# Kernel tuning notes

Hardware: AMD Instinct MI355X
Metric: run time of the kernel (lower is better)

The kernel has to match this reference:

```python
import jax, jax.numpy as jnp
import numpy as np

B, S, C = 16, 720, 862      # batch, seq_len, enc_in
P = 24                      # highest_freq_period
PAD = 720                   # seq_len % P == 0 -> pad_len == seq_len (no padding branch taken)
LQ = PAD // P               # 30, per-branch subsequence length == conv channels
DM = 128                    # d_model (PECBlock hidden conv channels)
EL = 2                      # e_layers
PRED = 336                  # pred_len
EPS = 1e-5                  # RevIN eps


def setup_inputs() -> dict:
    key = jax.random.key(0)
    ks = jax.random.split(key, 6)
    x = jax.random.normal(ks[0], (B, S, C), jnp.float32)
    # per-layer, per-branch pointwise conv weights (kernel_size=1, no bias)
    W1 = jax.random.normal(ks[1], (EL, P, DM, LQ), jnp.float32) * 0.05   # conv1: LQ -> DM
    W2 = jax.random.normal(ks[2], (EL, P, LQ, DM), jnp.float32) * 0.05   # conv2: DM -> LQ
    proj_w = jax.random.normal(ks[3], (PRED, S), jnp.float32) * 0.02      # Linear(seq_len, pred_len)
    proj_b = jnp.zeros((PRED,), jnp.float32)
    rev_w = jnp.ones((C,), jnp.float32)    # RevIN affine weight
    rev_b = jnp.zeros((C,), jnp.float32)   # RevIN affine bias
    return dict(x=x, W1=W1, W2=W2, proj_w=proj_w, proj_b=proj_b, rev_w=rev_w, rev_b=rev_b)


def reference(x, W1, W2, proj_w, proj_b, rev_w, rev_b):
    # RevIN 'norm': stats over time dim (unbiased=False var), affine
    mean = jnp.mean(x, axis=1, keepdims=True)
    stdev = jnp.sqrt(jnp.var(x, axis=1, keepdims=True) + EPS)
    xn = (x - mean) / stdev * rev_w + rev_b

    # seq_len % P == 0 so pad_time_series is identity
    x_padded = xn
    # NOTE: original loop feeds x_padded into EVERY block (not chained),
    # so each iteration overwrites y; replicated faithfully.
    # Strided gather idx::P == reshape (B,C,LQ,P) and index last axis;
    # scatter reassembly y[:,:,idx::P]=... == reshape back from (B,C,LQ,P).
    xs = x_padded.transpose(0, 2, 1).reshape(B, C, LQ, P)  # (B,C,LQ,P)
    y = x_padded
    for l in range(EL):
        h = jax.nn.gelu(jnp.einsum('pdq,bcqp->pbdc', W1[l], xs), approximate=False)  # (P,B,DM,C)
        ys = jnp.einsum('pqd,pbdc->bcqp', W2[l], h)                                  # (B,C,LQ,P)
        y = ys.reshape(B, C, PAD).transpose(0, 2, 1)                                 # (B,PAD,C)

    # PredictedProjection: Linear over time dim
    out = jnp.einsum('ps,bsc->bpc', proj_w, y[:, :S, :]) + proj_b[None, :, None]  # (B,PRED,C)

    # RevIN 'denorm'
    out = (out - rev_b) / (rev_w + EPS * EPS)
    out = out * stdev + mean
    return out
```

## Files before the change

kernel.cpp:

```cpp
#include <hip/hip_runtime.h>
#include <math.h>

typedef __attribute__((ext_vector_type(8))) short bf16x8;
typedef __attribute__((ext_vector_type(4))) short short4v;
typedef __attribute__((ext_vector_type(4))) float f32x4;

#define NB 16
#define NS 720
#define NC 862
#define NP 24
#define NQ 30
#define NDM 128
#define NPRED 336
#define BC (NB*NC)
#define SCH 10
#define SLEN 72
#define KP 768
#define PBASE (4*BC)
#define WOFF_F (24*BC)
#define NCOL (NB*NC)

__device__ __forceinline__ short f2bf(float f) {
    union { float f; unsigned u; } v; v.f = f;
    unsigned r = v.u + 0x7FFFu + ((v.u >> 16) & 1u);
    return (short)(r >> 16);
}

__device__ __forceinline__ float gelu_f(float h) {
    float hc = fminf(fmaxf(h, -8.f), 8.f);
    float z2 = hc * hc;
    float zz = hc * (0.79788456f + 0.035677408f * z2);
    float e  = __expf(-2.f * zz);
    return h * __builtin_amdgcn_rcpf(1.f + e);
}

__device__ __forceinline__ void gl_lds16(const void* g, void* l) {
    __builtin_amdgcn_global_load_lds(
        (const __attribute__((address_space(1))) unsigned int*)g,
        (__attribute__((address_space(3))) unsigned int*)l, 16, 0, 0);
}

__global__ __launch_bounds__(256) void stats_partial_k(const float* __restrict__ x,
                                                       float* __restrict__ ws) {
    int b = blockIdx.x, ct = blockIdx.y, ch = blockIdx.z;
    int c = ct * 256 + threadIdx.x;
    if (c >= NC) return;
    const float* xp = x + ((size_t)b * NS + (size_t)ch * SLEN) * NC + c;
    float s = 0.f, sq = 0.f;
    #pragma unroll 4
    for (int i = 0; i < SLEN; ++i) {
        float v = xp[(size_t)i * NC];
        s += v; sq += v * v;
    }
    int idx = b * NC + c;
    float* ps = ws + PBASE;
    ps[(size_t)ch * BC + idx] = s;
    ps[(size_t)(SCH + ch) * BC + idx] = sq;
}

__global__ __launch_bounds__(256) void stats_final_k(float* __restrict__ ws,
                                                     const float* __restrict__ revw,
                                                     const float* __restrict__ revb) {
    int idx = blockIdx.x * 256 + threadIdx.x;
    if (idx >= BC) return;
    const float* ps = ws + PBASE;
    float s = 0.f, sq = 0.f;
    #pragma unroll
    for (int ch = 0; ch < SCH; ++ch) {
        s  += ps[(size_t)ch * BC + idx];
        sq += ps[(size_t)(SCH + ch) * BC + idx];
    }
    int c = idx % NC;
    float mean  = s * (1.f / NS);
    float var   = sq * (1.f / NS) - mean * mean;
    float stdev = sqrtf(var + 1e-5f);
    float rstd  = 1.f / stdev;
    float aw = revw[c] * rstd;
    float u  = stdev / (revw[c] + 1e-10f);
    ws[idx]          = aw;
    ws[BC + idx]     = revb[c] - mean * aw;
    ws[2 * BC + idx] = u;
    ws[3 * BC + idx] = mean - revb[c] * u;
}

__global__ __launch_bounds__(256) void wprep_k(const float* __restrict__ W1,
                                               const float* __restrict__ W2,
                                               unsigned short* __restrict__ W1FF,
                                               unsigned short* __restrict__ W2FF) {
    int p = blockIdx.x, tid = threadIdx.x;
    const float* w1 = W1 + (size_t)(NP + p) * NDM * NQ;
    const float* w2 = W2 + (size_t)(NP + p) * NQ * NDM;
    #pragma unroll
    for (int pass = 0; pass < 2; ++pass) {
        int s = pass * 256 + tid;
        int l = s & 63, lr = l & 15, lg = l >> 4;
        {
            int dt = s >> 6;
            int d = dt * 16 + lr;
            bf16x8 v;
            #pragma unroll
            for (int j = 0; j < 8; ++j) {
                int q = 8 * lg + j;
                v[j] = f2bf(q < NQ ? w1[d * NQ + q] : 0.f);
            }
            ((bf16x8*)(W1FF + (size_t)p * 4096))[s] = v;
        }
        {
            int g = s >> 6, mi = g >> 2, ks = g & 3;
            int q = mi * 16 + lr, k = ks * 32 + 8 * lg;
            bf16x8 v;
            #pragma unroll
            for (int j = 0; j < 8; ++j)
                v[j] = f2bf(q < NQ ? w2[q * NDM + k + j] : 0.f);
            ((bf16x8*)(W2FF + (size_t)p * 4096))[s] = v;
        }
    }
}

__global__ __launch_bounds__(256) void pwprep_k(const float* __restrict__ pw,
                                                unsigned short* __restrict__ PWPF) {
    int t = blockIdx.x * 256 + threadIdx.x;
    if (t >= 24 * 24 * 64) return;
    int l = t & 63, ks = (t >> 6) % 24, st = t / (24 * 64);
    int lr = l & 15, lg = l >> 4;
    int m = st * 16 + lr;
    bf16x8 v;
    #pragma unroll
    for (int j = 0; j < 8; ++j) {
        int q = 8 * lg + j;
        v[j] = f2bf((m < NPRED && q < NQ) ? pw[(size_t)m * NS + q * NP + ks] : 0.f);
    }
    ((bf16x8*)PWPF)[t] = v;
}

__global__ __launch_bounds__(256) void branch_k(const float* __restrict__ x,
        const unsigned short* __restrict__ W1FF, const unsigned short* __restrict__ W2FF,
        const float* __restrict__ ws, unsigned short* __restrict__ y_t) {
    __shared__ __align__(16) short XsB[4 * 64 * 8];
    __shared__ __align__(16) short HB [16 * 64 * 8];
    int tid = threadIdx.x;
    int c0 = blockIdx.x * 64;
    int p  = blockIdx.y;
    int b  = blockIdx.z;

    {
        int c  = tid & 63, kb = tid >> 6;
        int cg = c0 + c;
        bool cv = cg < NC;
        int ce = cv ? cg : NC - 1;
        float aw = ws[b * NC + ce];
        float bw = ws[BC + b * NC + ce];
        const float* xb = x + ((size_t)b * NS + p) * NC + ce;
        bf16x8 v;
        #pragma unroll
        for (int j = 0; j < 8; ++j) {
            int q = kb * 8 + j;
            float val = (q < NQ && cv) ? xb[(size_t)q * NP * NC] * aw + bw : 0.f;
            v[j] = f2bf(val);
        }
        *(bf16x8*)&XsB[(size_t)(kb * 64 + (c ^ kb)) * 8] = v;
    }

    int w = tid >> 6, l = tid & 63, lr = l & 15, lg = l >> 4;
    f32x4 zf = {0.f, 0.f, 0.f, 0.f};
    const bf16x8* w1p = (const bf16x8*)(W1FF + (size_t)p * 4096);
    const bf16x8* w2p = (const bf16x8*)(W2FF + (size_t)p * 4096);
    bf16x8 a0 = w1p[(2 * w) * 64 + l];
    bf16x8 a1 = w1p[(2 * w + 1) * 64 + l];

    __syncthreads();

    f32x4 hc[2][4];
    #pragma unroll
    for (int ni = 0; ni < 4; ++ni) {
        bf16x8 bfr = *(const bf16x8*)&XsB[(size_t)(lg * 64 + ((ni * 16 + lr) ^ lg)) * 8];
        hc[0][ni] = __builtin_amdgcn_mfma_f32_16x16x32_bf16(a0, bfr, zf, 0, 0, 0);
        hc[1][ni] = __builtin_amdgcn_mfma_f32_16x16x32_bf16(a1, bfr, zf, 0, 0, 0);
    }
    #pragma unroll
    for (int mi2 = 0; mi2 < 2; ++mi2) {
        int d0 = (2 * w + mi2) * 16 + 4 * lg;
        int kb = d0 >> 3, sub = d0 & 7;
        #pragma unroll
        for (int ni = 0; ni < 4; ++ni) {
            short4v v;
            #pragma unroll
            for (int r = 0; r < 4; ++r)
                v[r] = f2bf(gelu_f(hc[mi2][ni][r]));
            int col = ni * 16 + lr;
            *(short4v*)&HB[(size_t)(kb * 64 + (col ^ kb)) * 8 + sub] = v;
        }
    }
    __syncthreads();

    f32x4 yacc[2] = {zf, zf};
    #pragma unroll
    for (int ks = 0; ks < 4; ++ks) {
        int kb = ks * 4 + lg;
        bf16x8 hfr = *(const bf16x8*)&HB[(size_t)(kb * 64 + ((w * 16 + lr) ^ kb)) * 8];
        #pragma unroll
        for (int mi = 0; mi < 2; ++mi) {
            bf16x8 w2f = w2p[(mi * 4 + ks) * 64 + l];
            yacc[mi] = __builtin_amdgcn_mfma_f32_16x16x32_bf16(w2f, hfr, yacc[mi], 0, 0, 0);
        }
    }
    int cg2 = c0 + w * 16 + lr;
    if (cg2 < NC) {
        unsigned short* base = y_t + ((size_t)(b * NC + cg2)) * KP + p * 32;
        #pragma unroll
        for (int mi = 0; mi < 2; ++mi) {
            int q0 = mi * 16 + 4 * lg;
            short4v v;
            #pragma unroll
            for (int r = 0; r < 4; ++r)
                v[r] = (q0 + r < NQ) ? f2bf(yacc[mi][r]) : (short)0;
            *(short4v*)(base + q0) = v;
        }
    }
}

__global__ __launch_bounds__(256, 4) void proj_k(const unsigned short* __restrict__ PWPF,
        const float* __restrict__ pb, const float* __restrict__ ws,
        const unsigned short* __restrict__ y_t, float* __restrict__ out) {
    __shared__ __align__(16) short L[2][12 * 512];
    int tid = threadIdx.x;
    int w = tid >> 6, l = tid & 63, lr = l & 15, lg = l >> 4;
    int gn0 = blockIdx.x * 128;
    int m0  = blockIdx.y * 64;
    f32x4 zf = {0.f, 0.f, 0.f, 0.f};
    f32x4 acc[4][2];
    #pragma unroll
    for (int mi = 0; mi < 4; ++mi) { acc[mi][0] = zf; acc[mi][1] = zf; }

    int cgA = gn0 + (2 * w) * 16 + lr;      if (cgA > NCOL - 1) cgA = NCOL - 1;
    int cgB = gn0 + (2 * w + 1) * 16 + lr;  if (cgB > NCOL - 1) cgB = NCOL - 1;
    const unsigned short* bsrcA = y_t + (size_t)cgA * KP + lg * 8;
    const unsigned short* bsrcB = y_t + (size_t)cgB * KP + lg * 8;
    const unsigned short* asrc  = PWPF + ((size_t)(m0 / 16 + w) * 24) * 512 + (size_t)l * 8;

#define STAGE(BUF, KS) do {                                              \
        gl_lds16(asrc  + (size_t)(KS) * 512, &L[BUF][w * 512]);          \
        gl_lds16(bsrcA + (size_t)(KS) * 32,  &L[BUF][(4 + 2 * w) * 512]);\
        gl_lds16(bsrcB + (size_t)(KS) * 32,  &L[BUF][(5 + 2 * w) * 512]);\
    } while (0)

    STAGE(0, 0);
    __syncthreads();
    int cur = 0;
    for (int ks = 0; ks < 24; ++ks) {
        if (ks + 1 < 24) STAGE(cur ^ 1, ks + 1);
        const short* Lc = &L[cur][0];
        bf16x8 b0 = *(const bf16x8*)&Lc[(4 + 2 * w) * 512 + l * 8];
        bf16x8 b1 = *(const bf16x8*)&Lc[(5 + 2 * w) * 512 + l * 8];
        #pragma unroll
        for (int mi = 0; mi < 4; ++mi) {
            bf16x8 a = *(const bf16x8*)&Lc[mi * 512 + l * 8];
            acc[mi][0] = __builtin_amdgcn_mfma_f32_16x16x32_bf16(a, b0, acc[mi][0], 0, 0, 0);
            acc[mi][1] = __builtin_amdgcn_mfma_f32_16x16x32_bf16(a, b1, acc[mi][1], 0, 0, 0);
        }
        __syncthreads();
        cur ^= 1;
    }
#undef STAGE

    #pragma unroll
    for (int mi = 0; mi < 4; ++mi) {
        #pragma unroll
        for (int r = 0; r < 4; ++r) {
            int pr = m0 + mi * 16 + 4 * lg + r;
            if (pr >= NPRED) continue;
            float bias = pb[pr];
            #pragma unroll
            for (int nj = 0; nj < 2; ++nj) {
                int cg = gn0 + (2 * w + nj) * 16 + lr;
                if (cg >= NCOL) continue;
                int bb = cg / NC;
                int cc = cg - bb * NC;
                out[((size_t)bb * NPRED + pr) * NC + cc] =
                    (acc[mi][nj][r] + bias) * ws[2 * BC + cg] + ws[3 * BC + cg];
            }
        }
    }
}

extern "C" void kernel_launch(void* const* d_in, const int* in_sizes, int n_in,
                              void* d_out, int out_size, void* d_ws, size_t ws_size,
                              hipStream_t stream) {
    const float* x   = (const float*)d_in[0];
    const float* W1  = (const float*)d_in[1];
    const float* W2  = (const float*)d_in[2];
    const float* pw  = (const float*)d_in[3];
    const float* pb  = (const float*)d_in[4];
    const float* rw  = (const float*)d_in[5];
    const float* rb  = (const float*)d_in[6];
    float* out = (float*)d_out;
    float* ws  = (float*)d_ws;
    unsigned short* W1FF = (unsigned short*)(ws + WOFF_F);
    unsigned short* W2FF = W1FF + NP * 4096;
    unsigned short* PWPF = W2FF + NP * 4096;
    unsigned short* y_t  = PWPF + 24 * 24 * 64 * 8;

    stats_partial_k<<<dim3(NB, 4, SCH), 256, 0, stream>>>(x, ws);
    wprep_k<<<dim3(NP), 256, 0, stream>>>(W1, W2, W1FF, W2FF);
    pwprep_k<<<dim3((24 * 24 * 64 + 255) / 256), 256, 0, stream>>>(pw, PWPF);
    stats_final_k<<<dim3((BC + 255) / 256), 256, 0, stream>>>(ws, rw, rb);
    branch_k<<<dim3(14, NP, NB), 256, 0, stream>>>(x, W1FF, W2FF, ws, y_t);
    proj_k<<<dim3((NCOL + 127) / 128, 6), 256, 0, stream>>>(PWPF, pb, ws, y_t, out);
}
```

Measured before the change: 83.65 us.

## Enlarge projection GEMM tile to 128x128 and vectorize stats loads

The projection kernel moves from a 64x128 output tile per block to 128x128. Its four waves are arranged 2x2, each computing a 64x64 sub-tile with 16 MFMA accumulators, and the LDS double buffer grows to hold the extra A and B fragments. This halves the number of M blocks and raises fragment reuse per LDS read, which should cut redundant global loads of y_t, at the cost of more registers, lower occupancy (launch bound 3) and fewer blocks to spread over the CUs. Separately, the stats partial kernel now reads two channels per thread with float2 loads and stores, halving its grid's y dimension.

After: 85.62 us. 1.02x slower.

```diff
diff --git a/kernel.cpp b/kernel.cpp
--- a/kernel.cpp
+++ b/kernel.cpp
@@ -42,20 +42,21 @@
 
 __global__ __launch_bounds__(256) void stats_partial_k(const float* __restrict__ x,
                                                        float* __restrict__ ws) {
-    int b = blockIdx.x, ct = blockIdx.y, ch = blockIdx.z;
-    int c = ct * 256 + threadIdx.x;
-    if (c >= NC) return;
-    const float* xp = x + ((size_t)b * NS + (size_t)ch * SLEN) * NC + c;
-    float s = 0.f, sq = 0.f;
+    int b = blockIdx.x, half = blockIdx.y, ch = blockIdx.z;
+    int t = half * 256 + threadIdx.x;
+    if (t >= NC / 2) return;
+    const float2* xp = (const float2*)(x + ((size_t)b * NS + (size_t)ch * SLEN) * NC) + t;
+    float2 s = {0.f, 0.f}, sq = {0.f, 0.f};
     #pragma unroll 4
     for (int i = 0; i < SLEN; ++i) {
-        float v = xp[(size_t)i * NC];
-        s += v; sq += v * v;
-    }
-    int idx = b * NC + c;
+        float2 v = xp[(size_t)i * (NC / 2)];
+        s.x += v.x; s.y += v.y;
+        sq.x += v.x * v.x; sq.y += v.y * v.y;
+    }
+    int idx = b * NC + t * 2;
     float* ps = ws + PBASE;
-    ps[(size_t)ch * BC + idx] = s;
-    ps[(size_t)(SCH + ch) * BC + idx] = sq;
+    *(float2*)&ps[(size_t)ch * BC + idx] = s;
+    *(float2*)&ps[(size_t)(SCH + ch) * BC + idx] = sq;
 }
 
 __global__ __launch_bounds__(256) void stats_final_k(float* __restrict__ ws,
@@ -219,29 +220,33 @@
     }
 }
 
-__global__ __launch_bounds__(256, 4) void proj_k(const unsigned short* __restrict__ PWPF,
+__global__ __launch_bounds__(256, 3) void proj_k(const unsigned short* __restrict__ PWPF,
         const float* __restrict__ pb, const float* __restrict__ ws,
         const unsigned short* __restrict__ y_t, float* __restrict__ out) {
-    __shared__ __align__(16) short L[2][12 * 512];
+    __shared__ __align__(16) short L[2][16 * 512];
     int tid = threadIdx.x;
     int w = tid >> 6, l = tid & 63, lr = l & 15, lg = l >> 4;
-    int gn0 = blockIdx.x * 128;
-    int m0  = blockIdx.y * 64;
+    int wm = w >> 1, wn = w & 1;
+    int n0 = blockIdx.x * 128, m0 = blockIdx.y * 128;
     f32x4 zf = {0.f, 0.f, 0.f, 0.f};
-    f32x4 acc[4][2];
-    #pragma unroll
-    for (int mi = 0; mi < 4; ++mi) { acc[mi][0] = zf; acc[mi][1] = zf; }
-
-    int cgA = gn0 + (2 * w) * 16 + lr;      if (cgA > NCOL - 1) cgA = NCOL - 1;
-    int cgB = gn0 + (2 * w + 1) * 16 + lr;  if (cgB > NCOL - 1) cgB = NCOL - 1;
-    const unsigned short* bsrcA = y_t + (size_t)cgA * KP + lg * 8;
-    const unsigned short* bsrcB = y_t + (size_t)cgB * KP + lg * 8;
-    const unsigned short* asrc  = PWPF + ((size_t)(m0 / 16 + w) * 24) * 512 + (size_t)l * 8;
-
-#define STAGE(BUF, KS) do {                                              \
-        gl_lds16(asrc  + (size_t)(KS) * 512, &L[BUF][w * 512]);          \
-        gl_lds16(bsrcA + (size_t)(KS) * 32,  &L[BUF][(4 + 2 * w) * 512]);\
-        gl_lds16(bsrcB + (size_t)(KS) * 32,  &L[BUF][(5 + 2 * w) * 512]);\
+    f32x4 acc[4][4];
+    #pragma unroll
+    for (int mi = 0; mi < 4; ++mi)
+        #pragma unroll
+        for (int nj = 0; nj < 4; ++nj) acc[mi][nj] = zf;
+
+    int cB0 = n0 + w * 16 + lr;        if (cB0 > NCOL - 1) cB0 = NCOL - 1;
+    int cB1 = n0 + (w + 4) * 16 + lr;  if (cB1 > NCOL - 1) cB1 = NCOL - 1;
+    const unsigned short* sA0 = PWPF + ((size_t)(m0 / 16 + w) * 24) * 512 + (size_t)l * 8;
+    const unsigned short* sA1 = PWPF + ((size_t)(m0 / 16 + w + 4) * 24) * 512 + (size_t)l * 8;
+    const unsigned short* sB0 = y_t + (size_t)cB0 * KP + lg * 8;
+    const unsigned short* sB1 = y_t + (size_t)cB1 * KP + lg * 8;
+
+#define STAGE(BUF, KS) do {                                          \
+        gl_lds16(sA0 + (size_t)(KS) * 512, &L[BUF][(w) * 512]);      \
+        gl_lds16(sA1 + (size_t)(KS) * 512, &L[BUF][(w + 4) * 512]);  \
+        gl_lds16(sB0 + (size_t)(KS) * 32,  &L[BUF][(8 + w) * 512]);  \
+        gl_lds16(sB1 + (size_t)(KS) * 32,  &L[BUF][(12 + w) * 512]); \
     } while (0)
 
     STAGE(0, 0);
@@ -249,14 +254,17 @@
     int cur = 0;
     for (int ks = 0; ks < 24; ++ks) {
         if (ks + 1 < 24) STAGE(cur ^ 1, ks + 1);
-        const short* Lc = &L[cur][0];
-        bf16x8 b0 = *(const bf16x8*)&Lc[(4 + 2 * w) * 512 + l * 8];
-        bf16x8 b1 = *(const bf16x8*)&Lc[(5 + 2 * w) * 512 + l * 8];
+        const short* Lc = L[cur];
+        bf16x8 bfr[4];
+        #pragma unroll
+        for (int nj = 0; nj < 4; ++nj)
+            bfr[nj] = *(const bf16x8*)&Lc[(8 + wn * 4 + nj) * 512 + l * 8];
         #pragma unroll
         for (int mi = 0; mi < 4; ++mi) {
-            bf16x8 a = *(const bf16x8*)&Lc[mi * 512 + l * 8];
-            acc[mi][0] = __builtin_amdgcn_mfma_f32_16x16x32_bf16(a, b0, acc[mi][0], 0, 0, 0);
-            acc[mi][1] = __builtin_amdgcn_mfma_f32_16x16x32_bf16(a, b1, acc[mi][1], 0, 0, 0);
+            bf16x8 a = *(const bf16x8*)&Lc[(wm * 4 + mi) * 512 + l * 8];
+            #pragma unroll
+            for (int nj = 0; nj < 4; ++nj)
+                acc[mi][nj] = __builtin_amdgcn_mfma_f32_16x16x32_bf16(a, bfr[nj], acc[mi][nj], 0, 0, 0);
         }
         __syncthreads();
         cur ^= 1;
@@ -267,12 +275,12 @@
     for (int mi = 0; mi < 4; ++mi) {
         #pragma unroll
         for (int r = 0; r < 4; ++r) {
-            int pr = m0 + mi * 16 + 4 * lg + r;
+            int pr = m0 + wm * 64 + mi * 16 + 4 * lg + r;
             if (pr >= NPRED) continue;
             float bias = pb[pr];
             #pragma unroll
-            for (int nj = 0; nj < 2; ++nj) {
-                int cg = gn0 + (2 * w + nj) * 16 + lr;
+            for (int nj = 0; nj < 4; ++nj) {
+                int cg = n0 + (wn * 4 + nj) * 16 + lr;
                 if (cg >= NCOL) continue;
                 int bb = cg / NC;
                 int cc = cg - bb * NC;
@@ -300,10 +308,10 @@
     unsigned short* PWPF = W2FF + NP * 4096;
     unsigned short* y_t  = PWPF + 24 * 24 * 64 * 8;
 
-    stats_partial_k<<<dim3(NB, 4, SCH), 256, 0, stream>>>(x, ws);
+    stats_partial_k<<<dim3(NB, 2, SCH), 256, 0, stream>>>(x, ws);
     wprep_k<<<dim3(NP), 256, 0, stream>>>(W1, W2, W1FF, W2FF);
     pwprep_k<<<dim3((24 * 24 * 64 + 255) / 256), 256, 0, stream>>>(pw, PWPF);
     stats_final_k<<<dim3((BC + 255) / 256), 256, 0, stream>>>(ws, rw, rb);
     branch_k<<<dim3(14, NP, NB), 256, 0, stream>>>(x, W1FF, W2FF, ws, y_t);
-    proj_k<<<dim3((NCOL + 127) / 128, 6), 256, 0, stream>>>(PWPF, pb, ws, y_t, out);
-}
+    proj_k<<<dim3((NCOL + 127) / 128, 3), 256, 0, stream>>>(PWPF, pb, ws, y_t, out);
+}
```

## Widen branch kernel tiles, vectorize stats loads, use packed bf16 conversion

Applied to the files above, without the earlier changes.

The branch kernel now runs 512 threads over 128 channels per block, with each wave owning one 16-row slice of the hidden dimension. All W2 fragments are preloaded into registers, which cuts per-block weight traffic and block count. Stats partials read float2 pairs to halve load instructions, and the hardware v_cvt_pk_bf16_f32 instruction replaces the manual rounding. The GELU input clamp is removed, which saves ALU work but could let __expf overflow for large inputs; register pressure rises with the 8 preloaded W2 fragments.

After: 85.61 us. +2.3%, slower.

```diff
diff --git a/kernel.cpp b/kernel.cpp
--- a/kernel.cpp
+++ b/kernel.cpp
@@ -26,10 +26,15 @@
     return (short)(r >> 16);
 }
 
+__device__ __forceinline__ unsigned cvt_pk_bf16(float a, float b) {
+    unsigned r;
+    asm("v_cvt_pk_bf16_f32 %0, %1, %2" : "=v"(r) : "v"(a), "v"(b));
+    return r;
+}
+
 __device__ __forceinline__ float gelu_f(float h) {
-    float hc = fminf(fmaxf(h, -8.f), 8.f);
-    float z2 = hc * hc;
-    float zz = hc * (0.79788456f + 0.035677408f * z2);
+    float z2 = h * h;
+    float zz = h * (0.79788456f + 0.035677408f * z2);
     float e  = __expf(-2.f * zz);
     return h * __builtin_amdgcn_rcpf(1.f + e);
 }
@@ -42,20 +47,21 @@
 
 __global__ __launch_bounds__(256) void stats_partial_k(const float* __restrict__ x,
                                                        float* __restrict__ ws) {
-    int b = blockIdx.x, ct = blockIdx.y, ch = blockIdx.z;
-    int c = ct * 256 + threadIdx.x;
-    if (c >= NC) return;
-    const float* xp = x + ((size_t)b * NS + (size_t)ch * SLEN) * NC + c;
-    float s = 0.f, sq = 0.f;
+    int b = blockIdx.x, half = blockIdx.y, ch = blockIdx.z;
+    int t = half * 256 + threadIdx.x;
+    if (t >= NC / 2) return;
+    const float2* xp = (const float2*)(x + ((size_t)b * NS + (size_t)ch * SLEN) * NC) + t;
+    float2 s = {0.f, 0.f}, sq = {0.f, 0.f};
     #pragma unroll 4
     for (int i = 0; i < SLEN; ++i) {
-        float v = xp[(size_t)i * NC];
-        s += v; sq += v * v;
-    }
-    int idx = b * NC + c;
+        float2 v = xp[(size_t)i * (NC / 2)];
+        s.x += v.x; s.y += v.y;
+        sq.x += v.x * v.x; sq.y += v.y * v.y;
+    }
+    int idx = b * NC + t * 2;
     float* ps = ws + PBASE;
-    ps[(size_t)ch * BC + idx] = s;
-    ps[(size_t)(SCH + ch) * BC + idx] = sq;
+    *(float2*)&ps[(size_t)ch * BC + idx] = s;
+    *(float2*)&ps[(size_t)(SCH + ch) * BC + idx] = sq;
 }
 
 __global__ __launch_bounds__(256) void stats_final_k(float* __restrict__ ws,
@@ -133,62 +139,63 @@
     ((bf16x8*)PWPF)[t] = v;
 }
 
-__global__ __launch_bounds__(256) void branch_k(const float* __restrict__ x,
+__global__ __launch_bounds__(512, 4) void branch_k(const float* __restrict__ x,
         const unsigned short* __restrict__ W1FF, const unsigned short* __restrict__ W2FF,
         const float* __restrict__ ws, unsigned short* __restrict__ y_t) {
-    __shared__ __align__(16) short XsB[4 * 64 * 8];
-    __shared__ __align__(16) short HB [16 * 64 * 8];
+    __shared__ __align__(16) short XsB[4 * 128 * 8];
+    __shared__ __align__(16) short HB [16 * 128 * 8];
     int tid = threadIdx.x;
-    int c0 = blockIdx.x * 64;
+    int c0 = blockIdx.x * 128;
     int p  = blockIdx.y;
     int b  = blockIdx.z;
 
     {
-        int c  = tid & 63, kb = tid >> 6;
-        int cg = c0 + c;
-        bool cv = cg < NC;
-        int ce = cv ? cg : NC - 1;
+        int cS = tid & 127, kbS = tid >> 7;
+        int cgS = c0 + cS;
+        bool cv = cgS < NC;
+        int ce = cv ? cgS : NC - 1;
         float aw = ws[b * NC + ce];
         float bw = ws[BC + b * NC + ce];
         const float* xb = x + ((size_t)b * NS + p) * NC + ce;
-        bf16x8 v;
+        float xs[8];
         #pragma unroll
         for (int j = 0; j < 8; ++j) {
-            int q = kb * 8 + j;
-            float val = (q < NQ && cv) ? xb[(size_t)q * NP * NC] * aw + bw : 0.f;
-            v[j] = f2bf(val);
-        }
-        *(bf16x8*)&XsB[(size_t)(kb * 64 + (c ^ kb)) * 8] = v;
+            int q = kbS * 8 + j;
+            xs[j] = (q < NQ && cv) ? xb[(size_t)q * NP * NC] * aw + bw : 0.f;
+        }
+        unsigned u[4];
+        #pragma unroll
+        for (int i = 0; i < 4; ++i) u[i] = cvt_pk_bf16(xs[2 * i], xs[2 * i + 1]);
+        *(uint4*)&XsB[(size_t)(kbS * 128 + (cS ^ kbS)) * 8] = *(uint4*)u;
     }
 
     int w = tid >> 6, l = tid & 63, lr = l & 15, lg = l >> 4;
     f32x4 zf = {0.f, 0.f, 0.f, 0.f};
     const bf16x8* w1p = (const bf16x8*)(W1FF + (size_t)p * 4096);
     const bf16x8* w2p = (const bf16x8*)(W2FF + (size_t)p * 4096);
-    bf16x8 a0 = w1p[(2 * w) * 64 + l];
-    bf16x8 a1 = w1p[(2 * w + 1) * 64 + l];
+    bf16x8 a0 = w1p[w * 64 + l];
+    bf16x8 w2f[8];
+    #pragma unroll
+    for (int g = 0; g < 8; ++g) w2f[g] = w2p[g * 64 + l];
 
     __syncthreads();
 
-    f32x4 hc[2][4];
-    #pragma unroll
-    for (int ni = 0; ni < 4; ++ni) {
-        bf16x8 bfr = *(const bf16x8*)&XsB[(size_t)(lg * 64 + ((ni * 16 + lr) ^ lg)) * 8];
-        hc[0][ni] = __builtin_amdgcn_mfma_f32_16x16x32_bf16(a0, bfr, zf, 0, 0, 0);
-        hc[1][ni] = __builtin_amdgcn_mfma_f32_16x16x32_bf16(a1, bfr, zf, 0, 0, 0);
-    }
-    #pragma unroll
-    for (int mi2 = 0; mi2 < 2; ++mi2) {
-        int d0 = (2 * w + mi2) * 16 + 4 * lg;
+    f32x4 hc[8];
+    #pragma unroll
+    for (int ni = 0; ni < 8; ++ni) {
+        bf16x8 bfr = *(const bf16x8*)&XsB[(size_t)(lg * 128 + ((ni * 16 + lr) ^ lg)) * 8];
+        hc[ni] = __builtin_amdgcn_mfma_f32_16x16x32_bf16(a0, bfr, zf, 0, 0, 0);
+    }
+    {
+        int d0 = w * 16 + 4 * lg;
         int kb = d0 >> 3, sub = d0 & 7;
         #pragma unroll
-        for (int ni = 0; ni < 4; ++ni) {
-            short4v v;
-            #pragma unroll
-            for (int r = 0; r < 4; ++r)
-                v[r] = f2bf(gelu_f(hc[mi2][ni][r]));
+        for (int ni = 0; ni < 8; ++ni) {
+            unsigned u0 = cvt_pk_bf16(gelu_f(hc[ni][0]), gelu_f(hc[ni][1]));
+            unsigned u1 = cvt_pk_bf16(gelu_f(hc[ni][2]), gelu_f(hc[ni][3]));
             int col = ni * 16 + lr;
-            *(short4v*)&HB[(size_t)(kb * 64 + (col ^ kb)) * 8 + sub] = v;
+            unsigned* dst = (unsigned*)&HB[(size_t)(kb * 128 + (col ^ kb)) * 8 + sub];
+            dst[0] = u0; dst[1] = u1;
         }
     }
     __syncthreads();
@@ -197,12 +204,11 @@
     #pragma unroll
     for (int ks = 0; ks < 4; ++ks) {
         int kb = ks * 4 + lg;
-        bf16x8 hfr = *(const bf16x8*)&HB[(size_t)(kb * 64 + ((w * 16 + lr) ^ kb)) * 8];
-        #pragma unroll
-        for (int mi = 0; mi < 2; ++mi) {
-            bf16x8 w2f = w2p[(mi * 4 + ks) * 64 + l];
-            yacc[mi] = __builtin_amdgcn_mfma_f32_16x16x32_bf16(w2f, hfr, yacc[mi], 0, 0, 0);
-        }
+        bf16x8 hfr = *(const bf16x8*)&HB[(size_t)(kb * 128 + ((w * 16 + lr) ^ kb)) * 8];
+        #pragma unroll
+        for (int mi = 0; mi < 2; ++mi)
+            yacc[mi] = __builtin_amdgcn_mfma_f32_16x16x32_bf16(w2f[mi * 4 + ks], hfr,
+                                                              yacc[mi], 0, 0, 0);
     }
     int cg2 = c0 + w * 16 + lr;
     if (cg2 < NC) {
@@ -210,11 +216,10 @@
         #pragma unroll
         for (int mi = 0; mi < 2; ++mi) {
             int q0 = mi * 16 + 4 * lg;
-            short4v v;
-            #pragma unroll
-            for (int r = 0; r < 4; ++r)
-                v[r] = (q0 + r < NQ) ? f2bf(yacc[mi][r]) : (short)0;
-            *(short4v*)(base + q0) = v;
+            unsigned u0 = cvt_pk_bf16(yacc[mi][0], yacc[mi][1]);
+            unsigned u1 = (q0 + 2 < NQ) ? cvt_pk_bf16(yacc[mi][2], yacc[mi][3]) : 0u;
+            uint2 uv = make_uint2(u0, u1);
+            *(uint2*)(base + q0) = uv;
         }
     }
 }
@@ -249,7 +254,7 @@
     int cur = 0;
     for (int ks = 0; ks < 24; ++ks) {
         if (ks + 1 < 24) STAGE(cur ^ 1, ks + 1);
-        const short* Lc = &L[cur][0];
+        const short* Lc = L[cur];
         bf16x8 b0 = *(const bf16x8*)&Lc[(4 + 2 * w) * 512 + l * 8];
         bf16x8 b1 = *(const bf16x8*)&Lc[(5 + 2 * w) * 512 + l * 8];
         #pragma unroll
@@ -300,10 +305,10 @@
     unsigned short* PWPF = W2FF + NP * 4096;
     unsigned short* y_t  = PWPF + 24 * 24 * 64 * 8;
 
-    stats_partial_k<<<dim3(NB, 4, SCH), 256, 0, stream>>>(x, ws);
+    stats_partial_k<<<dim3(NB, 2, SCH), 256, 0, stream>>>(x, ws);
     wprep_k<<<dim3(NP), 256, 0, stream>>>(W1, W2, W1FF, W2FF);
     pwprep_k<<<dim3((24 * 24 * 64 + 255) / 256), 256, 0, stream>>>(pw, PWPF);
     stats_final_k<<<dim3((BC + 255) / 256), 256, 0, stream>>>(ws, rw, rb);
-    branch_k<<<dim3(14, NP, NB), 256, 0, stream>>>(x, W1FF, W2FF, ws, y_t);
+    branch_k<<<dim3(7, NP, NB), 512, 0, stream>>>(x, W1FF, W2FF, ws, y_t);
     proj_k<<<dim3((NCOL + 127) / 128, 6), 256, 0, stream>>>(PWPF, pb, ws, y_t, out);
 }
```
